# Optimization experiments

Measured on AMD Instinct MI355X. Metric: run time of the kernel, lower is better.

## Reference

```python
import jax, jax.numpy as jnp
import numpy as np

EMBED_DIM = 768
NUM_HEADS = 12
HEAD_DIM = EMBED_DIM // NUM_HEADS


def setup_inputs() -> dict:
    key = jax.random.key(0)
    k_x, k_qkv_w, k_qkv_b, k_pw, k_pb = jax.random.split(key, 5)
    B, S = 16, 1024
    scale = 1.0 / np.sqrt(EMBED_DIM)
    return {
        "x": jax.random.normal(k_x, (B, S, EMBED_DIM), dtype=jnp.float32),
        "qkv_w": jax.random.normal(k_qkv_w, (EMBED_DIM, 3 * EMBED_DIM), dtype=jnp.float32) * scale,
        "qkv_b": jax.random.normal(k_qkv_b, (3 * EMBED_DIM,), dtype=jnp.float32) * 0.02,
        "proj_w": jax.random.normal(k_pw, (EMBED_DIM, EMBED_DIM), dtype=jnp.float32) * scale,
        "proj_b": jax.random.normal(k_pb, (EMBED_DIM,), dtype=jnp.float32) * 0.02,
    }


def reference(x, qkv_w, qkv_b, proj_w, proj_b):
    B, S, E = x.shape
    H, D = NUM_HEADS, HEAD_DIM
    qkv = x @ qkv_w + qkv_b                      # [B, S, 3E]
    qkv = qkv.reshape(B, S, 3, H, D)
    qkv = jnp.transpose(qkv, (2, 0, 3, 1, 4))    # [3, B, H, S, D]
    q, k, v = qkv[0], qkv[1], qkv[2]
    scores = jnp.einsum("bhqd,bhkd->bhqk", q, k) / jnp.sqrt(jnp.float32(D))
    probs = jax.nn.softmax(scores, axis=-1)      # dropout is identity in eval
    attn = jnp.einsum("bhqk,bhkd->bhqd", probs, v)
    attn = jnp.transpose(attn, (0, 2, 1, 3)).reshape(B, S, E)
    return attn @ proj_w + proj_b
```

## Files before the change

kernel.cpp:

```cpp
#include <hip/hip_runtime.h>
#include <hip/hip_bf16.h>

typedef unsigned short u16;
typedef short s16x8 __attribute__((ext_vector_type(8)));
typedef float f32x4 __attribute__((ext_vector_type(4)));

#define EMB 768
#define NH 12
#define HD 64
#define BB 16
#define SS 1024
#define MTOK (BB*SS)
#define NQKV (3*EMB)
#define QSZ ((size_t)BB*NH*SS*HD)

#define GLOBAL_AS const __attribute__((address_space(1))) void*
#define LDS_AS __attribute__((address_space(3))) void*

#if __has_builtin(__builtin_amdgcn_exp2f)
#define EXP2(x) __builtin_amdgcn_exp2f(x)
#else
#define EXP2(x) exp2f(x)
#endif

__device__ __forceinline__ u16 f2bf(float f){
  unsigned u = __float_as_uint(f);
  u += 0x7FFFu + ((u >> 16) & 1u);
  return (u16)(u >> 16);
}
__device__ __forceinline__ u16 f2bf_trunc(float f){
  return (u16)(__float_as_uint(f) >> 16);
}
__device__ __forceinline__ f32x4 mfma16(s16x8 a, s16x8 b, f32x4 c){
  return __builtin_amdgcn_mfma_f32_16x16x32_bf16(a, b, c, 0, 0, 0);
}

#define NBA 12288
#define NBB 1728
#define NBC 576

__device__ __forceinline__ void transpose_body(
    u16 (*tile)[33], const float* __restrict__ in, u16* __restrict__ out,
    int R, int C, int bxi, int byi){
  int bx = bxi * 32, by = byi * 32;
  int tx = threadIdx.x & 31, ty = threadIdx.x >> 5;
  #pragma unroll
  for(int i = 0; i < 32; i += 8)
    tile[ty + i][tx] = f2bf(in[(size_t)(by + ty + i) * C + bx + tx]);
  __syncthreads();
  #pragma unroll
  for(int i = 0; i < 32; i += 8)
    out[(size_t)(bx + ty + i) * R + by + tx] = tile[tx][ty + i];
}

__global__ __launch_bounds__(256) void prep_kernel(
    const float4* __restrict__ x4, ushort4* __restrict__ xb4,
    const float* __restrict__ qkv_w, u16* __restrict__ qkv_wT,
    const float* __restrict__ proj_w, u16* __restrict__ proj_wT){
  __shared__ u16 tile[32][33];
  int bid = blockIdx.x;
  if(bid < NBA){
    int i = bid * 256 + threadIdx.x;
    float4 f = x4[i];
    ushort4 o;
    o.x = f2bf(f.x); o.y = f2bf(f.y); o.z = f2bf(f.z); o.w = f2bf(f.w);
    xb4[i] = o;
  } else if(bid < NBA + NBB){
    int bi = bid - NBA;
    transpose_body(tile, qkv_w, qkv_wT, EMB, NQKV, bi % (NQKV/32), bi / (NQKV/32));
  } else {
    int bi = bid - NBA - NBB;
    transpose_body(tile, proj_w, proj_wT, EMB, EMB, bi % (EMB/32), bi / (EMB/32));
  }
}

template<int MODE>
__device__ __forceinline__ void gemm_body(
    const u16* __restrict__ A, const u16* __restrict__ Bt,
    const float* __restrict__ bias,
    void* __restrict__ out0, u16* __restrict__ out1, u16* __restrict__ out2){
  const int K = 768;
  __shared__ u16 As[2][128*64];
  __shared__ u16 Bs[2][128*64];
  int tid = threadIdx.x;

  int gx = gridDim.x;
  int nwg = gx * gridDim.y;
  int L = blockIdx.y * gx + blockIdx.x;
  int nl = (L & 7) * (nwg >> 3) + (L >> 3);
  int m0 = (nl / gx) * 128, n0 = (nl % gx) * 128;

  int w = tid >> 6, lane = tid & 63, quad = lane >> 4, l15 = lane & 15;
  int wm = (w >> 1) * 64, wn = (w & 1) * 64;
  int rr = lane >> 3;
  int cp = lane & 7;
  f32x4 acc[4][4] = {};

  auto stage = [&](int p, int k0){
    #pragma unroll
    for(int it = 0; it < 4; ++it){
      int ci = it * 4 + w;
      int r  = ci * 8 + rr;
      int gc = (cp ^ (r & 7)) * 8;
      __builtin_amdgcn_global_load_lds(
          (GLOBAL_AS)(A + (size_t)(m0 + r) * K + k0 + gc),
          (LDS_AS)(As[p] + ci * 512 + lane * 8), 16, 0, 0);
      __builtin_amdgcn_global_load_lds(
          (GLOBAL_AS)(Bt + (size_t)(n0 + r) * K + k0 + gc),
          (LDS_AS)(Bs[p] + ci * 512 + lane * 8), 16, 0, 0);
    }
  };

  stage(0, 0);
  int p = 0;
  for(int k0 = 0; k0 < K; k0 += 64){
    __syncthreads();
    if(k0 + 64 < K) stage(p ^ 1, k0 + 64);
    #pragma unroll
    for(int kk = 0; kk < 2; kk++){
      s16x8 a[4], b[4];
      int ch = ((kk * 4 + quad) ^ (l15 & 7)) * 8;
      #pragma unroll
      for(int i = 0; i < 4; i++){
        a[i] = *(const s16x8*)&As[p][(wm + i*16 + l15) * 64 + ch];
        b[i] = *(const s16x8*)&Bs[p][(wn + i*16 + l15) * 64 + ch];
      }
      #pragma unroll
      for(int mt = 0; mt < 4; mt++)
        #pragma unroll
        for(int nt = 0; nt < 4; nt++)
          acc[mt][nt] = mfma16(a[mt], b[nt], acc[mt][nt]);
    }
    p ^= 1;
  }

  #pragma unroll
  for(int mt = 0; mt < 4; mt++){
    #pragma unroll
    for(int nt = 0; nt < 4; nt++){
      int n = n0 + wn + nt*16 + l15;
      float bv = bias[n];
      #pragma unroll
      for(int r = 0; r < 4; r++){
        int m = m0 + wm + mt*16 + quad*4 + r;
        float v = acc[mt][nt][r] + bv;
        if(MODE == 1){
          ((float*)out0)[(size_t)m * EMB + n] = v;
        } else {
          u16 hv = f2bf(v);
          int which = n / EMB, rem = n - which * EMB;
          int h = rem >> 6, d = rem & 63;
          int b = m >> 10, s = m & 1023;
          size_t bh = (size_t)(b * NH + h);
          if(which == 0)      ((u16*)out0)[(bh * SS + s) * HD + d] = hv;
          else if(which == 1) out1[(bh * SS + s) * HD + d] = hv;
          else                out2[(bh * HD + d) * SS + s] = hv;
        }
      }
    }
  }
}

__global__ __launch_bounds__(256) void qkv_gemm_kernel(
    const u16* __restrict__ A, const u16* __restrict__ Bt,
    const float* __restrict__ bias,
    u16* __restrict__ Qo, u16* __restrict__ Ko, u16* __restrict__ Vo){
  gemm_body<0>(A, Bt, bias, Qo, Ko, Vo);
}
__global__ __launch_bounds__(256) void proj_gemm_kernel(
    const u16* __restrict__ A, const u16* __restrict__ Bt,
    const float* __restrict__ bias, float* __restrict__ out){
  gemm_body<1>(A, Bt, bias, out, nullptr, nullptr);
}

__global__ __launch_bounds__(256) void attn_kernel(
    const u16* __restrict__ Qws, const u16* __restrict__ Kws,
    const u16* __restrict__ Vtws, u16* __restrict__ attn){
  __shared__ u16 Ks[2][64*64];
  __shared__ u16 Vs[2][64*64];
  __shared__ __align__(16) u16 Ps[4][2][16][76];
  int tid = threadIdx.x;
  int w = tid >> 6, lane = tid & 63, quad = lane >> 4, l15 = lane & 15;
  int bh = blockIdx.x;
  int b = bh / NH, h = bh - b * NH;
  int q0 = blockIdx.y * 128 + w * 32;
  const u16* Qbase = Qws  + (size_t)bh * SS * HD;
  const u16* Kbase = Kws  + (size_t)bh * SS * HD;
  const u16* Vbase = Vtws + (size_t)bh * HD * SS;

  s16x8 aq[2][2];
  #pragma unroll
  for(int m = 0; m < 2; m++){
    int qrow = q0 + m*16 + l15;
    #pragma unroll
    for(int kk = 0; kk < 2; kk++)
      aq[m][kk] = *(const s16x8*)(Qbase + (size_t)qrow * HD + kk*32 + quad*8);
  }

  f32x4 o[2][4] = {};
  float psum[2][4] = {};
  const float C1 = 0.125f * 1.44269504f;
  const float C0 = -30.0f * 1.44269504f;

  int krr = lane >> 3, kcp = lane & 7;

  auto stageKV = [&](int p, int kt){
    #pragma unroll
    for(int it = 0; it < 2; ++it){
      int ins = it * 4 + w;
      int r   = ins * 8 + krr;
      int gck = (kcp ^ (r & 7)) * 8;
      __builtin_amdgcn_global_load_lds(
          (GLOBAL_AS)(Kbase + (size_t)(kt*64 + r) * HD + gck),
          (LDS_AS)(Ks[p] + ins * 512 + lane * 8), 16, 0, 0);
      __builtin_amdgcn_global_load_lds(
          (GLOBAL_AS)(Vbase + (size_t)r * SS + kt*64 + gck),
          (LDS_AS)(Vs[p] + ins * 512 + lane * 8), 16, 0, 0);
    }
  };

  stageKV(0, 0);
  int p = 0;
  for(int kt = 0; kt < 16; ++kt){
    __syncthreads();
    if(kt < 15) stageKV(p ^ 1, kt + 1);

    #pragma unroll
    for(int nt = 0; nt < 4; ++nt){
      s16x8 bk[2];
      #pragma unroll
      for(int kk = 0; kk < 2; kk++){
        int ch = ((kk*4 + quad) ^ (l15 & 7)) * 8;
        bk[kk] = *(const s16x8*)&Ks[p][(nt*16 + l15) * 64 + ch];
      }
      #pragma unroll
      for(int m = 0; m < 2; m++){
        f32x4 z = {};
        z = mfma16(aq[m][0], bk[0], z);
        z = mfma16(aq[m][1], bk[1], z);
        #pragma unroll
        for(int r = 0; r < 4; r++){
          float pv = EXP2(z[r] * C1 + C0);
          psum[m][r] += pv;
          Ps[w][m][quad*4 + r][nt*16 + l15] = f2bf_trunc(pv);
        }
      }
    }
    #pragma unroll
    for(int k4 = 0; k4 < 2; k4++){
      s16x8 pa[2];
      #pragma unroll
      for(int m = 0; m < 2; m++)
        pa[m] = *(const s16x8*)&Ps[w][m][l15][k4*32 + quad*8];
      #pragma unroll
      for(int nt = 0; nt < 4; nt++){
        int ch = ((k4*4 + quad) ^ (l15 & 7)) * 8;
        s16x8 vb = *(const s16x8*)&Vs[p][(nt*16 + l15) * 64 + ch];
        #pragma unroll
        for(int m = 0; m < 2; m++)
          o[m][nt] = mfma16(pa[m], vb, o[m][nt]);
      }
    }
    p ^= 1;
  }

  #pragma unroll
  for(int m = 0; m < 2; m++){
    #pragma unroll
    for(int r = 0; r < 4; r++){
      float s = psum[m][r];
      s += __shfl_xor(s, 1, 64);
      s += __shfl_xor(s, 2, 64);
      s += __shfl_xor(s, 4, 64);
      s += __shfl_xor(s, 8, 64);
      float inv = 1.0f / s;
      int srow = q0 + m*16 + quad*4 + r;
      size_t base = ((size_t)(b * SS + srow)) * EMB + h * HD;
      #pragma unroll
      for(int nt = 0; nt < 4; nt++)
        attn[base + nt*16 + l15] = f2bf(o[m][nt][r] * inv);
    }
  }
}

extern "C" void kernel_launch(void* const* d_in, const int* in_sizes, int n_in,
                              void* d_out, int out_size, void* d_ws, size_t ws_size,
                              hipStream_t stream){
  const float* x      = (const float*)d_in[0];
  const float* qkv_w  = (const float*)d_in[1];
  const float* qkv_b  = (const float*)d_in[2];
  const float* proj_w = (const float*)d_in[3];
  const float* proj_b = (const float*)d_in[4];

  char* ws = (char*)d_ws;
  u16* qkv_wT  = (u16*)ws; ws += (size_t)NQKV * EMB * 2;
  u16* proj_wT = (u16*)ws; ws += (size_t)EMB * EMB * 2;
  u16* x_bf = (u16*)ws; ws += QSZ * 2;
  u16* Qws  = (u16*)ws; ws += QSZ * 2;
  u16* Kws  = (u16*)ws; ws += QSZ * 2;
  u16* Vtws = (u16*)ws; ws += QSZ * 2;
  u16* attn = x_bf;

  prep_kernel<<<NBA + NBB + NBC, 256, 0, stream>>>(
      (const float4*)x, (ushort4*)x_bf, qkv_w, qkv_wT, proj_w, proj_wT);
  qkv_gemm_kernel<<<dim3(NQKV/128, MTOK/128), 256, 0, stream>>>(
      x_bf, qkv_wT, qkv_b, Qws, Kws, Vtws);
  attn_kernel<<<dim3(BB*NH, SS/128), 256, 0, stream>>>(Qws, Kws, Vtws, attn);
  proj_gemm_kernel<<<dim3(EMB/128, MTOK/128), 256, 0, stream>>>(
      attn, proj_wT, proj_b, (float*)d_out);
}
```

Before: 315.3 us.

## Enlarge GEMM tiles to 256x256 with 8 waves and deeper prefetch pipeline

Both GEMMs move from 128x128 tiles with 4 waves to 256x256 tiles with 8 waves, each wave computing 128x64, which doubles operand reuse per LDS load. The K loop is fully unrolled and split into phases. Loads are staged two tiles ahead with explicit vmcnt waits and split barriers, and s_setprio brackets the MFMA bursts. In exchange, LDS use doubles to 128KB, register pressure rises, and the grid gets smaller: 48x... for QKV and only 192 workgroups for the projection, which may underfill the GPU.

After: 314.9 us. No clear change (-0.1%).

```diff
diff --git a/kernel.cpp b/kernel.cpp
--- a/kernel.cpp
+++ b/kernel.cpp
@@ -79,69 +79,87 @@
     const u16* __restrict__ A, const u16* __restrict__ Bt,
     const float* __restrict__ bias,
     void* __restrict__ out0, u16* __restrict__ out1, u16* __restrict__ out2){
-  const int K = 768;
-  __shared__ u16 As[2][128*64];
-  __shared__ u16 Bs[2][128*64];
+  const int K = 768, NT = 12;
+  __shared__ u16 As[2][256*64];
+  __shared__ u16 Bs[2][256*64];
   int tid = threadIdx.x;
 
   int gx = gridDim.x;
   int nwg = gx * gridDim.y;
   int L = blockIdx.y * gx + blockIdx.x;
   int nl = (L & 7) * (nwg >> 3) + (L >> 3);
-  int m0 = (nl / gx) * 128, n0 = (nl % gx) * 128;
+  int m0 = (nl / gx) * 256, n0 = (nl % gx) * 256;
 
   int w = tid >> 6, lane = tid & 63, quad = lane >> 4, l15 = lane & 15;
-  int wm = (w >> 1) * 64, wn = (w & 1) * 64;
+  int wm = (w >> 2) * 128, wn = (w & 3) * 64;
   int rr = lane >> 3;
   int cp = lane & 7;
-  f32x4 acc[4][4] = {};
-
-  auto stage = [&](int p, int k0){
+  f32x4 acc[8][4] = {};
+
+  auto stage = [&](int t){
+    int d = t & 1, k0 = t * 64;
     #pragma unroll
     for(int it = 0; it < 4; ++it){
-      int ci = it * 4 + w;
+      int ci = it * 8 + w;
       int r  = ci * 8 + rr;
       int gc = (cp ^ (r & 7)) * 8;
       __builtin_amdgcn_global_load_lds(
           (GLOBAL_AS)(A + (size_t)(m0 + r) * K + k0 + gc),
-          (LDS_AS)(As[p] + ci * 512 + lane * 8), 16, 0, 0);
+          (LDS_AS)(As[d] + ci * 512 + lane * 8), 16, 0, 0);
       __builtin_amdgcn_global_load_lds(
           (GLOBAL_AS)(Bt + (size_t)(n0 + r) * K + k0 + gc),
-          (LDS_AS)(Bs[p] + ci * 512 + lane * 8), 16, 0, 0);
+          (LDS_AS)(Bs[d] + ci * 512 + lane * 8), 16, 0, 0);
     }
   };
 
-  stage(0, 0);
-  int p = 0;
-  for(int k0 = 0; k0 < K; k0 += 64){
-    __syncthreads();
-    if(k0 + 64 < K) stage(p ^ 1, k0 + 64);
-    #pragma unroll
-    for(int kk = 0; kk < 2; kk++){
-      s16x8 a[4], b[4];
+  stage(0); stage(1);
+  asm volatile("s_waitcnt vmcnt(8)" ::: "memory");
+  __builtin_amdgcn_s_barrier();
+
+  s16x8 a[4], b[4];
+  #pragma unroll
+  for(int t = 0; t < NT; ++t){
+    int d = t & 1;
+    #pragma unroll
+    for(int ph = 0; ph < 4; ++ph){
+      int kk = ph >> 1, mh = ph & 1;
       int ch = ((kk * 4 + quad) ^ (l15 & 7)) * 8;
-      #pragma unroll
-      for(int i = 0; i < 4; i++){
-        a[i] = *(const s16x8*)&As[p][(wm + i*16 + l15) * 64 + ch];
-        b[i] = *(const s16x8*)&Bs[p][(wn + i*16 + l15) * 64 + ch];
-      }
-      #pragma unroll
-      for(int mt = 0; mt < 4; mt++)
+      if(mh == 0){
         #pragma unroll
-        for(int nt = 0; nt < 4; nt++)
-          acc[mt][nt] = mfma16(a[mt], b[nt], acc[mt][nt]);
-    }
-    p ^= 1;
-  }
-
-  #pragma unroll
-  for(int mt = 0; mt < 4; mt++){
-    #pragma unroll
-    for(int nt = 0; nt < 4; nt++){
+        for(int nt = 0; nt < 4; ++nt)
+          b[nt] = *(const s16x8*)&Bs[d][(wn + nt*16 + l15) * 64 + ch];
+      }
+      #pragma unroll
+      for(int i = 0; i < 4; ++i)
+        a[i] = *(const s16x8*)&As[d][(wm + (mh*4 + i)*16 + l15) * 64 + ch];
+      __builtin_amdgcn_s_setprio(1);
+      #pragma unroll
+      for(int i = 0; i < 4; ++i)
+        #pragma unroll
+        for(int nt = 0; nt < 4; ++nt)
+          acc[mh*4 + i][nt] = mfma16(a[i], b[nt], acc[mh*4 + i][nt]);
+      __builtin_amdgcn_s_setprio(0);
+    }
+    if(t < NT - 1){
+      __builtin_amdgcn_s_barrier();
+      if(t + 2 < NT){
+        stage(t + 2);
+        asm volatile("s_waitcnt vmcnt(8)" ::: "memory");
+      } else {
+        asm volatile("s_waitcnt vmcnt(0)" ::: "memory");
+      }
+      __builtin_amdgcn_s_barrier();
+    }
+  }
+
+  #pragma unroll
+  for(int mt = 0; mt < 8; ++mt){
+    #pragma unroll
+    for(int nt = 0; nt < 4; ++nt){
       int n = n0 + wn + nt*16 + l15;
       float bv = bias[n];
       #pragma unroll
-      for(int r = 0; r < 4; r++){
+      for(int r = 0; r < 4; ++r){
         int m = m0 + wm + mt*16 + quad*4 + r;
         float v = acc[mt][nt][r] + bv;
         if(MODE == 1){
@@ -150,24 +168,24 @@
           u16 hv = f2bf(v);
           int which = n / EMB, rem = n - which * EMB;
           int h = rem >> 6, d = rem & 63;
-          int b = m >> 10, s = m & 1023;
-          size_t bh = (size_t)(b * NH + h);
-          if(which == 0)      ((u16*)out0)[(bh * SS + s) * HD + d] = hv;
-          else if(which == 1) out1[(bh * SS + s) * HD + d] = hv;
-          else                out2[(bh * HD + d) * SS + s] = hv;
+          int bb = m >> 10, ss = m & 1023;
+          size_t bh = (size_t)(bb * NH + h);
+          if(which == 0)      ((u16*)out0)[(bh * SS + ss) * HD + d] = hv;
+          else if(which == 1) out1[(bh * SS + ss) * HD + d] = hv;
+          else                out2[(bh * HD + d) * SS + ss] = hv;
         }
       }
     }
   }
 }
 
-__global__ __launch_bounds__(256) void qkv_gemm_kernel(
+__global__ __launch_bounds__(512, 2) void qkv_gemm_kernel(
     const u16* __restrict__ A, const u16* __restrict__ Bt,
     const float* __restrict__ bias,
     u16* __restrict__ Qo, u16* __restrict__ Ko, u16* __restrict__ Vo){
   gemm_body<0>(A, Bt, bias, Qo, Ko, Vo);
 }
-__global__ __launch_bounds__(256) void proj_gemm_kernel(
+__global__ __launch_bounds__(512, 2) void proj_gemm_kernel(
     const u16* __restrict__ A, const u16* __restrict__ Bt,
     const float* __restrict__ bias, float* __restrict__ out){
   gemm_body<1>(A, Bt, bias, out, nullptr, nullptr);
@@ -303,9 +321,9 @@
 
   prep_kernel<<<NBA + NBB + NBC, 256, 0, stream>>>(
       (const float4*)x, (ushort4*)x_bf, qkv_w, qkv_wT, proj_w, proj_wT);
-  qkv_gemm_kernel<<<dim3(NQKV/128, MTOK/128), 256, 0, stream>>>(
+  qkv_gemm_kernel<<<dim3(NQKV/256, MTOK/256), 512, 0, stream>>>(
       x_bf, qkv_wT, qkv_b, Qws, Kws, Vtws);
   attn_kernel<<<dim3(BB*NH, SS/128), 256, 0, stream>>>(Qws, Kws, Vtws, attn);
-  proj_gemm_kernel<<<dim3(EMB/128, MTOK/128), 256, 0, stream>>>(
+  proj_gemm_kernel<<<dim3(EMB/256, MTOK/256), 512, 0, stream>>>(
       attn, proj_wT, proj_b, (float*)d_out);
 }
```
